# Kernel tuning notes

Measured on AMD Instinct MI355X. Metric: run time of the kernel, lower is better.

Reference implementation:

```python
import jax, jax.numpy as jnp
import numpy as np
import math

B, S, HID = 16, 512, 768
NUM_LABELS = 9
NUM_HEADS = 4
HEAD_DIM = HID // NUM_HEADS
MAX_REL = 5
B_PERSON = 1
I_PERSON = 2
LN_EPS = 1e-5


def setup_inputs() -> dict:
    key = jax.random.key(0)
    ks = jax.random.split(key, 16)
    w = lambda k, shp: jax.random.normal(k, shp, dtype=jnp.float32) * 0.02
    return {
        "sequence_output": jax.random.normal(ks[0], (B, S, HID), dtype=jnp.float32),
        "Wq": w(ks[1], (HID, HID)), "bq": jnp.zeros((HID,), jnp.float32),
        "Wk": w(ks[2], (HID, HID)), "bk": jnp.zeros((HID,), jnp.float32),
        "Wv": w(ks[3], (HID, HID)), "bv": jnp.zeros((HID,), jnp.float32),
        "Wo": w(ks[4], (HID, HID)), "bo": jnp.zeros((HID,), jnp.float32),
        "ln_g": jnp.ones((HID,), jnp.float32), "ln_b": jnp.zeros((HID,), jnp.float32),
        "Ws": w(ks[5], (HID, NUM_LABELS)), "bs": jnp.zeros((NUM_LABELS,), jnp.float32),
        "entity_bias": w(ks[6], (NUM_LABELS,)),
    }


def _heads(x):
    # [B,S,HID] -> [B,H,S,D]
    return x.reshape(B, S, NUM_HEADS, HEAD_DIM).transpose(0, 2, 1, 3)


def reference(sequence_output, Wq, bq, Wk, bk, Wv, bv, Wo, bo, ln_g, ln_b, Ws, bs, entity_bias):
    x = sequence_output
    q = _heads(x @ Wq + bq)
    k = _heads(x @ Wk + bk)
    v = _heads(x @ Wv + bv)

    scores = jnp.einsum("bhqd,bhkd->bhqk", q, k)
    # relative position bias: exp(-0.1 * clamp(|i-j|, 0, MAX_REL)), broadcast over b,h
    idx = jnp.arange(S, dtype=jnp.float32)
    dist = jnp.abs(idx[None, :] - idx[:, None])  # [S,S]
    rel_bias = jnp.exp(-0.1 * jnp.clip(dist, 0.0, float(MAX_REL)))
    dist_mask = -0.1 * dist
    scores = (scores + rel_bias) / math.sqrt(HEAD_DIM) + dist_mask
    probs = jax.nn.softmax(scores, axis=-1)  # dropout is identity in eval

    ctx = jnp.einsum("bhqk,bhkd->bhqd", probs, v)
    ctx = ctx.transpose(0, 2, 1, 3).reshape(B, S, HID)
    out = ctx @ Wo + bo

    h = x + out
    mu = jnp.mean(h, axis=-1, keepdims=True)
    var = jnp.mean(jnp.square(h - mu), axis=-1, keepdims=True)
    h = (h - mu) * jax.lax.rsqrt(var + LN_EPS) * ln_g + ln_b

    span_logits = h @ Ws + bs  # [B,S,L]
    # vectorized entity-bias post-process: the torch loop adds entity_bias[I_PERSON]
    # TWICE to final_logits[:, j, I_PERSON] whenever argmax(span_logits[:, j-1]) == B_PERSON
    prev_is_b = jnp.argmax(span_logits[:, :-1], axis=-1) == B_PERSON  # [B,S-1]
    bump = jnp.where(prev_is_b, 2.0 * entity_bias[I_PERSON], 0.0)
    final_logits = span_logits.at[:, 1:, I_PERSON].add(bump)
    return final_logits
```

## Files before the change

kernel.cpp:

```cpp
#include <hip/hip_runtime.h>
#include <math.h>

#define SEQ 512
#define HID 768
#define NBATCH 16
#define ROWS 8192
#define INV_SQRT_D 0.07216878364870323f

typedef short s8v __attribute__((ext_vector_type(8)));
typedef _Float16 h8v __attribute__((ext_vector_type(8)));
typedef float f4v __attribute__((ext_vector_type(4)));
typedef unsigned short u16;

__device__ __forceinline__ u16 f2h(float f) {
  _Float16 h = (_Float16)f;
  return __builtin_bit_cast(u16, h);
}
__device__ __forceinline__ float h2f(u16 u) {
  return (float)__builtin_bit_cast(_Float16, u);
}

__device__ __forceinline__ void llds16(const u16* g, u16* l) {
  __builtin_amdgcn_global_load_lds(
      (const __attribute__((address_space(1))) void*)g,
      (__attribute__((address_space(3))) void*)l, 16, 0, 0);
}

template <int KSTEPS>
__device__ __forceinline__ void mm_core128(
    const u16* __restrict__ A, const int lda,
    const u16* __restrict__ B, const int ldb,
    u16* lds, f4v (&acc)[4][4])
{
  const int tid = threadIdx.x;
  const int w = tid >> 6, ln = tid & 63;
  const u16* src = (w >> 1) ? B : A;
  const int ld = (w >> 1) ? ldb : lda;
  const int half = w & 1;
  const int srow = ln >> 2;
  const int csw  = ((ln & 3) - (ln >> 3)) & 3;
  const int ml = ln & 15;
  const int fo2 = (((ln >> 4) + ((ln >> 1) & 3)) & 3) * 8;
  const int wr = (w >> 1) * 64, wc = (w & 1) * 64;

  const u16* gp[4];
  u16* lp[4];
#pragma unroll
  for (int t = 0; t < 4; ++t) {
    const int row = half * 64 + t * 16 + srow;
    gp[t] = src + (size_t)row * ld + csw * 8;
    lp[t] = lds + (w >> 1) * 4096 + half * 2048 + t * 512;
  }

  for (int kp = 0; kp < KSTEPS / 2; ++kp) {
    const int k0 = kp * 64;
    __syncthreads();
#pragma unroll
    for (int t = 0; t < 4; ++t) {
      llds16(gp[t] + k0,      lp[t]);
      llds16(gp[t] + k0 + 32, lp[t] + 8192);
    }
    __syncthreads();
#pragma unroll
    for (int sub = 0; sub < 2; ++sub) {
      const int so = sub * 8192;
      h8v a[4], b[4];
#pragma unroll
      for (int i = 0; i < 4; ++i)
        a[i] = *(const h8v*)&lds[so + (wr + i * 16 + ml) * 32 + fo2];
#pragma unroll
      for (int j = 0; j < 4; ++j)
        b[j] = *(const h8v*)&lds[so + 4096 + (wc + j * 16 + ml) * 32 + fo2];
#pragma unroll
      for (int i = 0; i < 4; ++i)
#pragma unroll
        for (int j = 0; j < 4; ++j)
          acc[i][j] = __builtin_amdgcn_mfma_f32_16x16x32_f16(a[i], b[j], acc[i][j], 0, 0, 0);
    }
  }
}

__global__ __launch_bounds__(256) void splitx(const float* __restrict__ x,
                                              u16* __restrict__ xh)
{
  const int i = blockIdx.x * 256 + threadIdx.x;
  const float4 v = ((const float4*)x)[i];
  ((ushort4*)xh)[i] = make_ushort4(f2h(v.x), f2h(v.y), f2h(v.z), f2h(v.w));
}

__global__ __launch_bounds__(256) void wsplit(
    const float* __restrict__ Wq, const float* __restrict__ Wk,
    const float* __restrict__ Wv, const float* __restrict__ Wo,
    u16* __restrict__ WTh)
{
  __shared__ float t[32][33];
  const int z = blockIdx.z;
  const float* W = (z == 0) ? Wq : (z == 1) ? Wk : (z == 2) ? Wv : Wo;
  const int n0 = blockIdx.x * 32, k0 = blockIdx.y * 32;
  const int tx = threadIdx.x & 31, ty = threadIdx.x >> 5;
#pragma unroll
  for (int i = 0; i < 4; ++i)
    t[ty + 8 * i][tx] = W[(size_t)(k0 + ty + 8 * i) * HID + n0 + tx];
  __syncthreads();
#pragma unroll
  for (int i = 0; i < 4; ++i) {
    const float v = t[tx][ty + 8 * i];
    const size_t idx = (size_t)z * HID * HID + (size_t)(n0 + ty + 8 * i) * HID + k0 + tx;
    WTh[idx] = f2h(v);
  }
}

__global__ __launch_bounds__(256, 4) void qkv_mm(
    const u16* __restrict__ xh, const u16* __restrict__ WTh,
    const float* __restrict__ bq, const float* __restrict__ bk, const float* __restrict__ bv,
    u16* __restrict__ qh, u16* __restrict__ kh, u16* __restrict__ vTh)
{
  __shared__ u16 lds[18432];
  const int id = blockIdx.x;
  const int xcd = id & 7;
  const int s = id >> 3;
  const int bx = s % 6;
  const int yl = (s / 6) & 7;
  const int z  = s / 48;
  const int bm = (yl * 8 + xcd) * 128;
  const int bn = bx * 128;
  const size_t wtoff = (size_t)z * HID * HID + (size_t)bn * HID;
  f4v acc[4][4];
#pragma unroll
  for (int i = 0; i < 4; ++i)
#pragma unroll
    for (int j = 0; j < 4; ++j) acc[i][j] = (f4v)0.f;
  mm_core128<24>(xh + (size_t)bm * HID, HID, WTh + wtoff, HID, lds, acc);
  const int tid = threadIdx.x, w = tid >> 6, ln = tid & 63;
  const int ml = ln & 15, quad = ln >> 4;
  const int wr = (w >> 1) * 64, wc = (w & 1) * 64;
  if (z == 2) {
    __syncthreads();
#pragma unroll
    for (int i = 0; i < 4; ++i)
#pragma unroll
      for (int j = 0; j < 4; ++j) {
        const int ncol = wc + j * 16 + ml;
        const float bv_ = bv[bn + ncol];
#pragma unroll
        for (int r = 0; r < 4; ++r) {
          const int srow = wr + i * 16 + quad * 4 + r;
          lds[ncol * 136 + srow] = f2h(acc[i][j][r] + bv_);
        }
      }
    __syncthreads();
    u16* vb = vTh + (size_t)(bm >> 9) * HID * SEQ;
    const int sq0 = bm & 511;
    const int c8 = (tid & 15) * 8;
#pragma unroll
    for (int p = 0; p < 8; ++p) {
      const int nl = p * 16 + (tid >> 4);
      const s8v val = *(const s8v*)&lds[nl * 136 + c8];
      *(s8v*)&vb[(size_t)(bn + nl) * SEQ + sq0 + c8] = val;
    }
  } else {
    const float* bias = (z == 0) ? bq : bk;
    u16* dst = (z == 0) ? qh : kh;
    __syncthreads();
#pragma unroll
    for (int i = 0; i < 4; ++i)
#pragma unroll
      for (int j = 0; j < 4; ++j) {
        const int col = wc + j * 16 + ml;
        const float bv_ = bias[bn + col];
#pragma unroll
        for (int r = 0; r < 4; ++r) {
          const int row = wr + i * 16 + quad * 4 + r;
          lds[row * 132 + col] = f2h(acc[i][j][r] + bv_);
        }
      }
    __syncthreads();
    const int c8 = (tid & 15) * 8;
#pragma unroll
    for (int p = 0; p < 8; ++p) {
      const int rl = p * 16 + (tid >> 4);
      const s8v val = *(const s8v*)&lds[rl * 132 + c8];
      *(s8v*)&dst[(size_t)(bm + rl) * HID + bn + c8] = val;
    }
  }
}

__global__ __launch_bounds__(256, 2) void attn_fused(
    const u16* __restrict__ qh, const u16* __restrict__ kh,
    const u16* __restrict__ vTh, u16* __restrict__ ch)
{
  __shared__ u16 lds[29184];
  __shared__ float gtab[1024];
  __shared__ float red[4][32];
  const int f = blockIdx.x;
  const int xcd = f & 7, s = f >> 3;
  const int z = xcd * 8 + (s >> 3);
  const int bm = (s & 7) * 64;
  const int b = z >> 2, hh = z & 3;
  const int tid = threadIdx.x, w = tid >> 6, ln = tid & 63;
  const int ml = ln & 15, quad = ln >> 4;
  const int rh = w >> 1, ch2 = w & 1;
  const int fo2 = ((quad + ((ml >> 1) & 3)) & 3) * 8;

  for (int t = tid; t < 1023; t += 256) {
    const float fd = fabsf((float)(t - 511));
    gtab[t] = INV_SQRT_D * __expf(-0.1f * fminf(fd, 5.0f)) - 0.1f * fd;
  }

  const u16* qbase = qh + (size_t)(b * SEQ + bm + rh * 32) * HID + hh * 192;
  const u16* kbase = kh + (size_t)b * SEQ * HID + hh * 192;
  const u16* vbase = vTh + (size_t)b * HID * SEQ + (size_t)(hh * 192) * SEQ;

  h8v qf[2][6];
#pragma unroll
  for (int i = 0; i < 2; ++i)
#pragma unroll
    for (int ks = 0; ks < 6; ++ks)
      qf[i][ks] = *(const h8v*)(qbase + (size_t)(i * 16 + ml) * HID + ks * 32 + quad * 8);

  const int srow16 = ln >> 2;
  const int csw = ((ln & 3) - (ln >> 3)) & 3;
  const u16* ksrc = kbase + (size_t)(w * 16 + srow16) * HID + csw * 8;
  const u16* vsrc = vbase + (size_t)(w * 48 + srow16) * SEQ + csw * 8;

  f4v acc2[2][6];
#pragma unroll
  for (int i = 0; i < 2; ++i)
#pragma unroll
    for (int jj = 0; jj < 6; ++jj) acc2[i][jj] = (f4v)0.f;
  float rsum[2][4];
#pragma unroll
  for (int i = 0; i < 2; ++i)
#pragma unroll
    for (int r = 0; r < 4; ++r) rsum[i][r] = 0.f;

  for (int j = 0; j < 8; ++j) {
    __syncthreads();
#pragma unroll
    for (int st = 0; st < 6; ++st)
      llds16(ksrc + (size_t)(j * 64) * HID + st * 32, lds + st * 2048 + w * 512);
#pragma unroll
    for (int st = 0; st < 2; ++st)
#pragma unroll
      for (int o = 0; o < 3; ++o)
        llds16(vsrc + (size_t)(o * 16) * SEQ + j * 64 + st * 32,
               lds + 12288 + st * 6144 + w * 1536 + o * 512);
    __syncthreads();
    f4v sacc[2][2];
    sacc[0][0] = (f4v)0.f; sacc[0][1] = (f4v)0.f;
    sacc[1][0] = (f4v)0.f; sacc[1][1] = (f4v)0.f;
    __builtin_amdgcn_s_setprio(1);
#pragma unroll
    for (int ks = 0; ks < 6; ++ks) {
      h8v kf0 = *(const h8v*)&lds[ks * 2048 + (ch2 * 32 + ml) * 32 + fo2];
      h8v kf1 = *(const h8v*)&lds[ks * 2048 + (ch2 * 32 + 16 + ml) * 32 + fo2];
      sacc[0][0] = __builtin_amdgcn_mfma_f32_16x16x32_f16(qf[0][ks], kf0, sacc[0][0], 0, 0, 0);
      sacc[1][0] = __builtin_amdgcn_mfma_f32_16x16x32_f16(qf[1][ks], kf0, sacc[1][0], 0, 0, 0);
      sacc[0][1] = __builtin_amdgcn_mfma_f32_16x16x32_f16(qf[0][ks], kf1, sacc[0][1], 0, 0, 0);
      sacc[1][1] = __builtin_amdgcn_mfma_f32_16x16x32_f16(qf[1][ks], kf1, sacc[1][1], 0, 0, 0);
    }
    __builtin_amdgcn_s_setprio(0);
#pragma unroll
    for (int i = 0; i < 2; ++i)
#pragma unroll
      for (int j2 = 0; j2 < 2; ++j2) {
        const int lcol = ch2 * 32 + j2 * 16 + ml;
        const int scolg = j * 64 + lcol;
#pragma unroll
        for (int r = 0; r < 4; ++r) {
          const int lrow = rh * 32 + i * 16 + quad * 4 + r;
          const float g = gtab[bm + lrow - scolg + 511];
          const float p = __expf(fmaf(sacc[i][j2][r], INV_SQRT_D, g));
          rsum[i][r] += p;
          lds[24576 + lrow * 72 + lcol] = f2h(p);
        }
      }
    __syncthreads();
    __builtin_amdgcn_s_setprio(1);
#pragma unroll
    for (int ks = 0; ks < 2; ++ks) {
      h8v pf[2], vf[6];
#pragma unroll
      for (int i = 0; i < 2; ++i)
        pf[i] = *(const h8v*)&lds[24576 + (rh * 32 + i * 16 + ml) * 72 + ks * 32 + quad * 8];
#pragma unroll
      for (int jj = 0; jj < 6; ++jj)
        vf[jj] = *(const h8v*)&lds[12288 + ks * 6144 + (ch2 * 96 + jj * 16 + ml) * 32 + fo2];
#pragma unroll
      for (int i = 0; i < 2; ++i)
#pragma unroll
        for (int jj = 0; jj < 6; ++jj)
          acc2[i][jj] = __builtin_amdgcn_mfma_f32_16x16x32_f16(pf[i], vf[jj], acc2[i][jj], 0, 0, 0);
    }
    __builtin_amdgcn_s_setprio(0);
  }

#pragma unroll
  for (int i = 0; i < 2; ++i)
#pragma unroll
    for (int r = 0; r < 4; ++r) {
      float t = rsum[i][r];
#pragma unroll
      for (int o = 1; o < 16; o <<= 1) t += __shfl_xor(t, o, 64);
      rsum[i][r] = t;
    }
  if (ml == 0) {
#pragma unroll
    for (int i = 0; i < 2; ++i)
#pragma unroll
      for (int r = 0; r < 4; ++r) red[w][i * 16 + quad * 4 + r] = rsum[i][r];
  }
  __syncthreads();

#pragma unroll
  for (int i = 0; i < 2; ++i)
#pragma unroll
    for (int r = 0; r < 4; ++r) {
      const int lr = i * 16 + quad * 4 + r;
      const float is = 1.0f / (red[rh * 2][lr] + red[rh * 2 + 1][lr]);
      const int m = bm + rh * 32 + lr;
#pragma unroll
      for (int jj = 0; jj < 6; ++jj) {
        const int gcol = hh * 192 + ch2 * 96 + jj * 16 + ml;
        ch[(size_t)(b * SEQ + m) * HID + gcol] = f2h(acc2[i][jj][r] * is);
      }
    }
}

__global__ __launch_bounds__(256, 4) void proj_mm(
    const u16* __restrict__ ch, const u16* __restrict__ WTh,
    const float* __restrict__ bo, const u16* __restrict__ xh, u16* __restrict__ hh)
{
  __shared__ u16 lds[18432];
  const int id = blockIdx.x;
  const int xcd = id & 7;
  const int s = id >> 3;
  const int bx = s % 6;
  const int yl = s / 6;
  const int bm = (yl * 8 + xcd) * 128;
  const int bn = bx * 128;
  const size_t wtoff = (size_t)3 * HID * HID + (size_t)bn * HID;
  f4v acc[4][4];
#pragma unroll
  for (int i = 0; i < 4; ++i)
#pragma unroll
    for (int j = 0; j < 4; ++j) acc[i][j] = (f4v)0.f;
  mm_core128<24>(ch + (size_t)bm * HID, HID, WTh + wtoff, HID, lds, acc);
  const int tid = threadIdx.x, w = tid >> 6, ln = tid & 63;
  const int ml = ln & 15, quad = ln >> 4;
  const int wr = (w >> 1) * 64, wc = (w & 1) * 64;
  __syncthreads();
#pragma unroll
  for (int i = 0; i < 4; ++i)
#pragma unroll
    for (int j = 0; j < 4; ++j) {
      const int col = wc + j * 16 + ml;
      const float bv_ = bo[bn + col];
#pragma unroll
      for (int r = 0; r < 4; ++r) {
        const int row = wr + i * 16 + quad * 4 + r;
        lds[row * 132 + col] = f2h(acc[i][j][r] + bv_);
      }
    }
  __syncthreads();
  const int c8 = (tid & 15) * 8;
#pragma unroll
  for (int p = 0; p < 8; ++p) {
    const int rl = p * 16 + (tid >> 4);
    const size_t goff = (size_t)(bm + rl) * HID + bn + c8;
    const h8v ov = __builtin_bit_cast(h8v, *(const s8v*)&lds[rl * 132 + c8]);
    const h8v xv = __builtin_bit_cast(h8v, *(const s8v*)&xh[goff]);
    const h8v sum = ov + xv;
    *(s8v*)&hh[goff] = __builtin_bit_cast(s8v, sum);
  }
}

__global__ __launch_bounds__(256) void ln_logits_kernel(
    const u16* __restrict__ hh, const float* __restrict__ g,
    const float* __restrict__ bta, const float* __restrict__ Ws,
    const float* __restrict__ bsv, float* __restrict__ span)
{
  const int row = blockIdx.x * 4 + (threadIdx.x >> 6);
  const int lane = threadIdx.x & 63;
  const u16* hr = hh + (size_t)row * HID;
  float v[3][4];
#pragma unroll
  for (int sgm = 0; sgm < 3; ++sgm) {
    const ushort4 raw = *(const ushort4*)&hr[sgm * 256 + lane * 4];
    v[sgm][0] = h2f(raw.x); v[sgm][1] = h2f(raw.y);
    v[sgm][2] = h2f(raw.z); v[sgm][3] = h2f(raw.w);
  }
  float s = 0.f, sq = 0.f;
#pragma unroll
  for (int sgm = 0; sgm < 3; ++sgm)
#pragma unroll
    for (int e = 0; e < 4; ++e) { s += v[sgm][e]; sq += v[sgm][e] * v[sgm][e]; }
#pragma unroll
  for (int o = 1; o < 64; o <<= 1) { s += __shfl_xor(s, o, 64); sq += __shfl_xor(sq, o, 64); }
  const float mu = s / 768.0f;
  const float rs = rsqrtf(sq / 768.0f - mu * mu + 1e-5f);
  float pl[9];
#pragma unroll
  for (int l = 0; l < 9; ++l) pl[l] = 0.f;
#pragma unroll
  for (int sgm = 0; sgm < 3; ++sgm) {
    const int c0 = sgm * 256 + lane * 4;
    const float4 gg = ((const float4*)g)[sgm * 64 + lane];
    const float4 bb = ((const float4*)bta)[sgm * 64 + lane];
    const float n0 = (v[sgm][0] - mu) * rs * gg.x + bb.x;
    const float n1 = (v[sgm][1] - mu) * rs * gg.y + bb.y;
    const float n2 = (v[sgm][2] - mu) * rs * gg.z + bb.z;
    const float n3 = (v[sgm][3] - mu) * rs * gg.w + bb.w;
    const float* w0 = Ws + (size_t)c0 * 9;
#pragma unroll
    for (int l = 0; l < 9; ++l)
      pl[l] += n0 * w0[l] + n1 * w0[9 + l] + n2 * w0[18 + l] + n3 * w0[27 + l];
  }
#pragma unroll
  for (int l = 0; l < 9; ++l)
#pragma unroll
    for (int o = 1; o < 64; o <<= 1) pl[l] += __shfl_xor(pl[l], o, 64);
  if (lane == 0) {
    float* sp = span + (size_t)row * 9;
#pragma unroll
    for (int l = 0; l < 9; ++l) sp[l] = pl[l] + bsv[l];
  }
}

__global__ __launch_bounds__(256) void bump_kernel(
    const float* __restrict__ span, const float* __restrict__ eb, float* __restrict__ out)
{
  const int idx = blockIdx.x * 256 + threadIdx.x;
  if (idx >= ROWS) return;
  const int j = idx & (SEQ - 1);
  const float* sl = span + (size_t)idx * 9;
  float v[9];
#pragma unroll
  for (int l = 0; l < 9; ++l) v[l] = sl[l];
  if (j >= 1) {
    const float* sp = sl - 9;
    float m = sp[0]; int am = 0;
#pragma unroll
    for (int l = 1; l < 9; ++l) { const float t = sp[l]; if (t > m) { m = t; am = l; } }
    if (am == 1) v[2] += 2.0f * eb[2];
  }
#pragma unroll
  for (int l = 0; l < 9; ++l) out[(size_t)idx * 9 + l] = v[l];
}

extern "C" void kernel_launch(void* const* d_in, const int* in_sizes, int n_in,
                              void* d_out, int out_size, void* d_ws, size_t ws_size,
                              hipStream_t stream)
{
  (void)in_sizes; (void)n_in; (void)out_size; (void)ws_size;
  const float* x   = (const float*)d_in[0];
  const float* Wq  = (const float*)d_in[1];
  const float* bq  = (const float*)d_in[2];
  const float* Wk  = (const float*)d_in[3];
  const float* bk  = (const float*)d_in[4];
  const float* Wv  = (const float*)d_in[5];
  const float* bv  = (const float*)d_in[6];
  const float* Wo  = (const float*)d_in[7];
  const float* bo  = (const float*)d_in[8];
  const float* lng = (const float*)d_in[9];
  const float* lnb = (const float*)d_in[10];
  const float* Ws  = (const float*)d_in[11];
  const float* bs  = (const float*)d_in[12];
  const float* eb  = (const float*)d_in[13];
  float* out = (float*)d_out;

  char* ws = (char*)d_ws;
  u16* xh  = (u16*)(ws + 0);
  u16* WTh = (u16*)(ws + 25165824);
  u16* qh  = (u16*)(ws + 34603008);
  u16* kh  = (u16*)(ws + 59768832);
  u16* vTh = (u16*)(ws + 84934656);
  u16* hh  = (u16*)(ws + 110100480);
  float* spanb = (float*)(ws + 152043520);
  u16* ctxh = qh;

  splitx<<<dim3(1572864 / 256), 256, 0, stream>>>(x, xh);
  wsplit<<<dim3(24, 24, 4), 256, 0, stream>>>(Wq, Wk, Wv, Wo, WTh);
  qkv_mm<<<dim3(1152), 256, 0, stream>>>(xh, WTh, bq, bk, bv, qh, kh, vTh);
  attn_fused<<<dim3(512), 256, 0, stream>>>(qh, kh, vTh, ctxh);
  proj_mm<<<dim3(384), 256, 0, stream>>>(ctxh, WTh, bo, xh, hh);
  ln_logits_kernel<<<dim3(ROWS / 4), 256, 0, stream>>>(hh, lng, lnb, Ws, bs, spanb);
  bump_kernel<<<dim3(ROWS / 256), 256, 0, stream>>>(spanb, eb, out);
}
```

Baseline: 198.4 us.

## Load V fragments directly into registers and merge input prep kernels

Two changes. First, the attention kernel no longer stages V tiles into LDS. Each wave loads its V^T fragments straight from global memory into registers, which shrinks shared memory and removes the LDS reads for V, at the cost of uncoalesced-ish global loads and more VGPRs. Second, the x fp16 conversion and the weight transpose-convert kernels are merged into a single launch, removing one kernel launch. The __syncthreads inside the weight branch is block-uniform, so it stays safe.

```diff
diff --git a/kernel.cpp b/kernel.cpp
--- a/kernel.cpp
+++ b/kernel.cpp
@@ -80,33 +80,35 @@
   }
 }
 
-__global__ __launch_bounds__(256) void splitx(const float* __restrict__ x,
-                                              u16* __restrict__ xh)
-{
-  const int i = blockIdx.x * 256 + threadIdx.x;
-  const float4 v = ((const float4*)x)[i];
-  ((ushort4*)xh)[i] = make_ushort4(f2h(v.x), f2h(v.y), f2h(v.z), f2h(v.w));
-}
-
-__global__ __launch_bounds__(256) void wsplit(
+__global__ __launch_bounds__(256) void prep_kernel(
+    const float* __restrict__ x,
     const float* __restrict__ Wq, const float* __restrict__ Wk,
     const float* __restrict__ Wv, const float* __restrict__ Wo,
-    u16* __restrict__ WTh)
+    u16* __restrict__ xh, u16* __restrict__ WTh)
 {
   __shared__ float t[32][33];
-  const int z = blockIdx.z;
-  const float* W = (z == 0) ? Wq : (z == 1) ? Wk : (z == 2) ? Wv : Wo;
-  const int n0 = blockIdx.x * 32, k0 = blockIdx.y * 32;
-  const int tx = threadIdx.x & 31, ty = threadIdx.x >> 5;
-#pragma unroll
-  for (int i = 0; i < 4; ++i)
-    t[ty + 8 * i][tx] = W[(size_t)(k0 + ty + 8 * i) * HID + n0 + tx];
-  __syncthreads();
-#pragma unroll
-  for (int i = 0; i < 4; ++i) {
-    const float v = t[tx][ty + 8 * i];
-    const size_t idx = (size_t)z * HID * HID + (size_t)(n0 + ty + 8 * i) * HID + k0 + tx;
-    WTh[idx] = f2h(v);
+  const int bid = blockIdx.x;
+  if (bid < 6144) {
+    const int i = bid * 256 + threadIdx.x;
+    const float4 v = ((const float4*)x)[i];
+    ((ushort4*)xh)[i] = make_ushort4(f2h(v.x), f2h(v.y), f2h(v.z), f2h(v.w));
+  } else {
+    const int wb = bid - 6144;
+    const int z = wb / 576;
+    const int r = wb % 576;
+    const int n0 = (r % 24) * 32, k0 = (r / 24) * 32;
+    const float* W = (z == 0) ? Wq : (z == 1) ? Wk : (z == 2) ? Wv : Wo;
+    const int tx = threadIdx.x & 31, ty = threadIdx.x >> 5;
+#pragma unroll
+    for (int i = 0; i < 4; ++i)
+      t[ty + 8 * i][tx] = W[(size_t)(k0 + ty + 8 * i) * HID + n0 + tx];
+    __syncthreads();
+#pragma unroll
+    for (int i = 0; i < 4; ++i) {
+      const float v = t[tx][ty + 8 * i];
+      const size_t idx = (size_t)z * HID * HID + (size_t)(n0 + ty + 8 * i) * HID + k0 + tx;
+      WTh[idx] = f2h(v);
+    }
   }
 }
 
@@ -189,7 +191,7 @@
     const u16* __restrict__ qh, const u16* __restrict__ kh,
     const u16* __restrict__ vTh, u16* __restrict__ ch)
 {
-  __shared__ u16 lds[29184];
+  __shared__ u16 lds[16896];
   __shared__ float gtab[1024];
   __shared__ float red[4][32];
   const int f = blockIdx.x;
@@ -221,7 +223,11 @@
   const int srow16 = ln >> 2;
   const int csw = ((ln & 3) - (ln >> 3)) & 3;
   const u16* ksrc = kbase + (size_t)(w * 16 + srow16) * HID + csw * 8;
-  const u16* vsrc = vbase + (size_t)(w * 48 + srow16) * SEQ + csw * 8;
+
+  const u16* vrow[6];
+#pragma unroll
+  for (int jj = 0; jj < 6; ++jj)
+    vrow[jj] = vbase + (size_t)(ch2 * 96 + jj * 16 + ml) * SEQ + quad * 8;
 
   f4v acc2[2][6];
 #pragma unroll
@@ -239,13 +245,13 @@
 #pragma unroll
     for (int st = 0; st < 6; ++st)
       llds16(ksrc + (size_t)(j * 64) * HID + st * 32, lds + st * 2048 + w * 512);
-#pragma unroll
-    for (int st = 0; st < 2; ++st)
-#pragma unroll
-      for (int o = 0; o < 3; ++o)
-        llds16(vsrc + (size_t)(o * 16) * SEQ + j * 64 + st * 32,
-               lds + 12288 + st * 6144 + w * 1536 + o * 512);
-    __syncthreads();
+    __syncthreads();
+    h8v vr[2][6];
+#pragma unroll
+    for (int ks = 0; ks < 2; ++ks)
+#pragma unroll
+      for (int jj = 0; jj < 6; ++jj)
+        vr[ks][jj] = *(const h8v*)(vrow[jj] + j * 64 + ks * 32);
     f4v sacc[2][2];
     sacc[0][0] = (f4v)0.f; sacc[0][1] = (f4v)0.f;
     sacc[1][0] = (f4v)0.f; sacc[1][1] = (f4v)0.f;
@@ -272,25 +278,22 @@
           const float g = gtab[bm + lrow - scolg + 511];
           const float p = __expf(fmaf(sacc[i][j2][r], INV_SQRT_D, g));
           rsum[i][r] += p;
-          lds[24576 + lrow * 72 + lcol] = f2h(p);
+          lds[12288 + lrow * 72 + lcol] = f2h(p);
         }
       }
     __syncthreads();
     __builtin_amdgcn_s_setprio(1);
 #pragma unroll
     for (int ks = 0; ks < 2; ++ks) {
-      h8v pf[2], vf[6];
+      h8v pf[2];
 #pragma unroll
       for (int i = 0; i < 2; ++i)
-        pf[i] = *(const h8v*)&lds[24576 + (rh * 32 + i * 16 + ml) * 72 + ks * 32 + quad * 8];
-#pragma unroll
-      for (int jj = 0; jj < 6; ++jj)
-        vf[jj] = *(const h8v*)&lds[12288 + ks * 6144 + (ch2 * 96 + jj * 16 + ml) * 32 + fo2];
+        pf[i] = *(const h8v*)&lds[12288 + (rh * 32 + i * 16 + ml) * 72 + ks * 32 + quad * 8];
 #pragma unroll
       for (int i = 0; i < 2; ++i)
 #pragma unroll
         for (int jj = 0; jj < 6; ++jj)
-          acc2[i][jj] = __builtin_amdgcn_mfma_f32_16x16x32_f16(pf[i], vf[jj], acc2[i][jj], 0, 0, 0);
+          acc2[i][jj] = __builtin_amdgcn_mfma_f32_16x16x32_f16(pf[i], vr[ks][jj], acc2[i][jj], 0, 0, 0);
     }
     __builtin_amdgcn_s_setprio(0);
   }
@@ -479,8 +482,7 @@
   float* spanb = (float*)(ws + 152043520);
   u16* ctxh = qh;
 
-  splitx<<<dim3(1572864 / 256), 256, 0, stream>>>(x, xh);
-  wsplit<<<dim3(24, 24, 4), 256, 0, stream>>>(Wq, Wk, Wv, Wo, WTh);
+  prep_kernel<<<dim3(8448), 256, 0, stream>>>(x, Wq, Wk, Wv, Wo, xh, WTh);
   qkv_mm<<<dim3(1152), 256, 0, stream>>>(xh, WTh, bq, bk, bv, qh, kh, vTh);
   attn_fused<<<dim3(512), 256, 0, stream>>>(qh, kh, vTh, ctxh);
   proj_mm<<<dim3(384), 256, 0, stream>>>(ctxh, WTh, bo, xh, hh);
```

Result: slower. 202.9 us (+2.2%).
